# Optimization experiments

Hardware: AMD Instinct MI355X
Metric: run time of the kernel (lower is better)

The kernel has to match this reference:

```python
import jax, jax.numpy as jnp
import numpy as np

H = W = 64          # input_resolution
C = 256             # dim
HEADS = 8
WS = 8              # window_size
SHIFT = WS // 2
DEPTH = 2           # block 0: no shift, block 1: shifted + mask
HIDDEN = 4 * C      # mlp_ratio * dim
B = 8
N = WS * WS                 # tokens per window
NW = (H // WS) * (W // WS)  # windows per image
EPS = 1e-5


def _rel_pos_index():
    coords = np.stack(np.meshgrid(np.arange(WS), np.arange(WS), indexing='ij')).reshape(2, -1)
    rel = (coords[:, :, None] - coords[:, None, :]).transpose(1, 2, 0)
    rel[:, :, 0] += WS - 1
    rel[:, :, 1] += WS - 1
    rel[:, :, 0] *= 2 * WS - 1
    return rel.sum(-1)  # [N, N] indices into (2*ws-1)^2 table

REL_IDX = jnp.asarray(_rel_pos_index())


def _attn_mask():
    # Swin shift mask: label 3x3 regions, compare window-token labels
    img = np.zeros((H, W))
    slices = (slice(0, -WS), slice(-WS, -SHIFT), slice(-SHIFT, None))
    cnt = 0
    for hs in slices:
        for ws_ in slices:
            img[hs, ws_] = cnt
            cnt += 1
    mw = img.reshape(H // WS, WS, W // WS, WS).transpose(0, 2, 1, 3).reshape(-1, N)
    diff = mw[:, None, :] - mw[:, :, None]
    return jnp.asarray(np.where(diff != 0, -100.0, 0.0), dtype=np.float32)  # [nW, N, N]

ATTN_MASK = _attn_mask()


def layernorm(x, g, b):
    mu = jnp.mean(x, axis=-1, keepdims=True)
    var = jnp.mean((x - mu) ** 2, axis=-1, keepdims=True)
    return (x - mu) * jax.lax.rsqrt(var + EPS) * g + b


def setup_inputs() -> dict:
    key = jax.random.key(0)
    ks = jax.random.split(key, 6)
    s = 0.02
    return {
        'x': jax.random.normal(ks[0], (B, H * W, C), jnp.float32),
        'qkv_w': jax.random.normal(ks[1], (DEPTH, C, 3 * C), jnp.float32) * s,
        'qkv_b': jnp.zeros((DEPTH, 3 * C), jnp.float32),
        'proj_w': jax.random.normal(ks[2], (DEPTH, C, C), jnp.float32) * s,
        'proj_b': jnp.zeros((DEPTH, C), jnp.float32),
        'ln1_g': jnp.ones((DEPTH, C), jnp.float32),
        'ln1_b': jnp.zeros((DEPTH, C), jnp.float32),
        'ln2_g': jnp.ones((DEPTH, C), jnp.float32),
        'ln2_b': jnp.zeros((DEPTH, C), jnp.float32),
        'fc1_w': jax.random.normal(ks[3], (DEPTH, C, HIDDEN), jnp.float32) * s,
        'fc1_b': jnp.zeros((DEPTH, HIDDEN), jnp.float32),
        'fc2_w': jax.random.normal(ks[4], (DEPTH, HIDDEN, C), jnp.float32) * s,
        'fc2_b': jnp.zeros((DEPTH, C), jnp.float32),
        'rpb': jax.random.normal(ks[5], (DEPTH, (2 * WS - 1) ** 2, HEADS), jnp.float32) * s,
    }


def window_attention(xw, qw, qb, pw, pb, rpb_i, mask):
    # xw: [B*nW, N, C]
    B_ = xw.shape[0]
    d = C // HEADS
    qkv = (xw @ qw + qb).reshape(B_, N, 3, HEADS, d).transpose(2, 0, 3, 1, 4)
    q, k, v = qkv[0] * (d ** -0.5), qkv[1], qkv[2]   # [B_, h, N, d]
    attn = jnp.einsum('bhnd,bhmd->bhnm', q, k)
    bias = rpb_i[REL_IDX.reshape(-1)].reshape(N, N, HEADS).transpose(2, 0, 1)
    attn = attn + bias[None]
    if mask is not None:
        attn = attn.reshape(-1, NW, HEADS, N, N) + mask[None, :, None]
        attn = attn.reshape(-1, HEADS, N, N)
    attn = jax.nn.softmax(attn, axis=-1)
    out = jnp.einsum('bhnm,bhmd->bhnd', attn, v).transpose(0, 2, 1, 3).reshape(B_, N, C)
    return out @ pw + pb


def reference(x, qkv_w, qkv_b, proj_w, proj_b, ln1_g, ln1_b, ln2_g, ln2_b,
              fc1_w, fc1_b, fc2_w, fc2_b, rpb):
    for i in range(DEPTH):
        shift = 0 if i % 2 == 0 else SHIFT
        mask = None if shift == 0 else ATTN_MASK
        shortcut = x
        h = layernorm(x, ln1_g[i], ln1_b[i]).reshape(-1, H, W, C)
        if shift:
            h = jnp.roll(h, (-shift, -shift), axis=(1, 2))
        # window partition -> [B*nW, N, C]
        hw = h.reshape(-1, H // WS, WS, W // WS, WS, C).transpose(0, 1, 3, 2, 4, 5).reshape(-1, N, C)
        aw = window_attention(hw, qkv_w[i], qkv_b[i], proj_w[i], proj_b[i], rpb[i], mask)
        # window reverse
        h = aw.reshape(-1, H // WS, W // WS, WS, WS, C).transpose(0, 1, 3, 2, 4, 5).reshape(-1, H, W, C)
        if shift:
            h = jnp.roll(h, (shift, shift), axis=(1, 2))
        x = shortcut + h.reshape(-1, H * W, C)
        m = layernorm(x, ln2_g[i], ln2_b[i])
        m = jax.nn.gelu(m @ fc1_w[i] + fc1_b[i], approximate=False) @ fc2_w[i] + fc2_b[i]
        x = x + m
    return x
```

## Files before the change

### kernel.cpp

```cpp
#include <hip/hip_runtime.h>
#include <hip/hip_bf16.h>


typedef __hip_bfloat16 bf16;
typedef unsigned short u16;
typedef unsigned int u32;
typedef short short8 __attribute__((ext_vector_type(8)));
typedef float floatx4 __attribute__((ext_vector_type(4)));

#define DEVI static __device__ __forceinline__
#define WAITCNT_VM(n) asm volatile("s_waitcnt vmcnt(" #n ")" ::: "memory")

DEVI float lo16(u32 u) { union { u32 i; float f; } x; x.i = u << 16; return x.f; }
DEVI float hi16(u32 u) { union { u32 i; float f; } x; x.i = u & 0xffff0000u; return x.f; }
DEVI float b2f(u16 u) { union { u32 i; float f; } x; x.i = ((u32)u) << 16; return x.f; }
DEVI u16 f2b(float f) {
  union { float f; u32 i; } x; x.f = f;
  u32 r = x.i + 0x7fffu + ((x.i >> 16) & 1u);
  return (u16)(r >> 16);
}
DEVI float in_elem(const void* p, size_t i, int m) {
  return m ? b2f(((const u16*)p)[i]) : ((const float*)p)[i];
}
DEVI int swlab(int g) { return (g < 56) ? 0 : (g < 60 ? 1 : 2); }

DEVI float gelu_cheap(float v) {
  const float u = v * v;
  const float t = v * __builtin_fmaf(0.1029436f, u, 2.3022090f);
  const float e = __builtin_amdgcn_exp2f(t);
  const float r = __builtin_amdgcn_rcpf(e + 1.0f);
  return __builtin_fmaf(-v, r, v);
}

DEVI void async16(const bf16* g, bf16* l) {
  __builtin_amdgcn_global_load_lds((const __attribute__((address_space(1))) u32*)g,
                                   (__attribute__((address_space(3))) u32*)l, 16, 0, 0);
}

__global__ void k_detect(const u32* __restrict__ ln1g, int* __restrict__ mode) {
  if (threadIdx.x == 0 && blockIdx.x == 0)
    *mode = (ln1g[0] == 0x3F803F80u) ? 1 : 0;
}

__global__ __launch_bounds__(256) void k_ingest_ln(const void* __restrict__ xin,
    float* __restrict__ xf, const void* __restrict__ gamw, const void* __restrict__ betw,
    bf16* __restrict__ outp, const int* __restrict__ mode)
{
  const int m = *mode;
  const int l = threadIdx.x & 63, w = threadIdx.x >> 6;
  const int row = blockIdx.x * 4 + w;
  const int t = row & 63, win = row >> 6;
  const int bb = win >> 6, wi = win & 63;
  const int gh = ((wi >> 3) << 3) + (t >> 3);
  const int gw = ((wi & 7) << 3) + (t & 7);
  const int srow = (bb << 12) + (gh << 6) + gw;
  const int cb = l << 2;
  float4 v;
  if (m) {
    const uint2 u = *(const uint2*)((const u16*)xin + (size_t)srow * 256 + cb);
    v = make_float4(lo16(u.x), hi16(u.x), lo16(u.y), hi16(u.y));
  } else {
    v = ((const float4*)((const float*)xin + (size_t)srow * 256))[l];
  }
  ((float4*)(xf + (size_t)srow * 256))[l] = v;
  float s = v.x + v.y + v.z + v.w;
#pragma unroll
  for (int off = 32; off > 0; off >>= 1) s += __shfl_xor(s, off, 64);
  const float mu = s * 0.00390625f;
  const float a = v.x - mu, b = v.y - mu, c = v.z - mu, d = v.w - mu;
  float q = a * a + b * b + c * c + d * d;
#pragma unroll
  for (int off = 32; off > 0; off >>= 1) q += __shfl_xor(q, off, 64);
  const float rs = rsqrtf(q * 0.00390625f + 1e-5f);
  const float o0 = a * rs * in_elem(gamw, cb + 0, m) + in_elem(betw, cb + 0, m);
  const float o1 = b * rs * in_elem(gamw, cb + 1, m) + in_elem(betw, cb + 1, m);
  const float o2 = c * rs * in_elem(gamw, cb + 2, m) + in_elem(betw, cb + 2, m);
  const float o3 = d * rs * in_elem(gamw, cb + 3, m) + in_elem(betw, cb + 3, m);
  const u32 p0 = (u32)f2b(o0) | ((u32)f2b(o1) << 16);
  const u32 p1 = (u32)f2b(o2) | ((u32)f2b(o3) << 16);
  *(uint2*)((u16*)outp + (size_t)row * 256 + cb) = make_uint2(p0, p1);
}

__global__ __launch_bounds__(256) void k_transpose(
    const void* __restrict__ src, bf16* __restrict__ dst,
    const int* __restrict__ mode, int estride, int dstride, int R, int Cn) {
  __shared__ float T[32][33];
  const int m = *mode;
  const int tx = threadIdx.x & 31, ty = threadIdx.x >> 5;
  const int bc = blockIdx.x << 5, br = blockIdx.y << 5;
  for (int d = 0; d < 2; ++d) {
    __syncthreads();
#pragma unroll
    for (int dy = 0; dy < 4; ++dy) {
      const int r = br + ty + dy * 8;
      T[ty + dy * 8][tx] = in_elem(src, (size_t)d * estride + (size_t)r * Cn + bc + tx, m);
    }
    __syncthreads();
#pragma unroll
    for (int dy = 0; dy < 4; ++dy) {
      const int c = bc + ty + dy * 8;
      ((u16*)dst)[(size_t)d * dstride + (size_t)c * R + br + tx] = f2b(T[tx][ty + dy * 8]);
    }
  }
}

template <int EPI>
__global__ __launch_bounds__(256, 3) void k_gemm(
    const bf16* __restrict__ A, const bf16* __restrict__ Bt,
    const void* __restrict__ bias, bf16* __restrict__ outb,
    const int* __restrict__ mode, int boff, int K, int N)
{
  __shared__ __align__(16) bf16 As[3][128 * 32];
  __shared__ __align__(16) bf16 Bs[3][128 * 32];
  __shared__ __align__(16) float EPs[4][4][72];
  const int md = *mode;
  const int tid = threadIdx.x;
  const int l = tid & 63, wid = tid >> 6;
  const int wr = wid >> 1, wc = wid & 1;

  const int gx = gridDim.x;
  const int nwg = gx * gridDim.y;
  int fid = blockIdx.y * gx + blockIdx.x;
  if (!(nwg & 7)) fid = (fid & 7) * (nwg >> 3) + (fid >> 3);
  const int row0 = (fid / gx) * 128;
  const int col0 = (fid % gx) * 128;

  const int lrow = l >> 2;
  const int lkof = (((l & 3) ^ ((l >> 3) & 3)) * 8);
  const int qsw  = (((l >> 4) ^ ((l >> 1) & 3)) * 8);

  floatx4 acc[4][4];
#pragma unroll
  for (int mi = 0; mi < 4; ++mi)
#pragma unroll
    for (int ni = 0; ni < 4; ++ni)
      acc[mi][ni] = (floatx4){0.f, 0.f, 0.f, 0.f};

  auto stage = [&](int b, int kbase) {
    const int kk = kbase + lkof;
#pragma unroll
    for (int c = 0; c < 2; ++c) {
      const int seg = c * 4 + wid;
      async16(A + (size_t)(row0 + seg * 16 + lrow) * K + kk, &As[b][seg * 512]);
      async16(Bt + (size_t)(col0 + seg * 16 + lrow) * K + kk, &Bs[b][seg * 512]);
    }
  };

  const int nsl = K >> 5;
  stage(0, 0);
  stage(1, 32);

  for (int s = 0; s < nsl; ++s) {
    const int cur = s % 3;
    if (s < nsl - 1) { WAITCNT_VM(4); }
    else            { WAITCNT_VM(0); }
    __builtin_amdgcn_s_barrier();
    if (s + 2 < nsl) stage((s + 2) % 3, (s + 2) * 32);

    short8 af[4], bq[4];
#pragma unroll
    for (int mi = 0; mi < 4; ++mi)
      af[mi] = *(const short8*)&As[cur][(wr * 64 + mi * 16 + (l & 15)) * 32 + qsw];
#pragma unroll
    for (int ni = 0; ni < 4; ++ni)
      bq[ni] = *(const short8*)&Bs[cur][(wc * 64 + ni * 16 + (l & 15)) * 32 + qsw];
#pragma unroll
    for (int mi = 0; mi < 4; ++mi)
#pragma unroll
      for (int ni = 0; ni < 4; ++ni)
        acc[mi][ni] = __builtin_amdgcn_mfma_f32_16x16x32_bf16(af[mi], bq[ni], acc[mi][ni], 0, 0, 0);
  }

  float* EPw = &EPs[wid][0][0];
  const int cl = l & 15, rq = l >> 4;
  const int colb = wc * 64 + cl * 4;
  float bias4[4];
#pragma unroll
  for (int i = 0; i < 4; ++i) bias4[i] = in_elem(bias, (size_t)boff + col0 + colb + i, md);

#pragma unroll
  for (int mi = 0; mi < 4; ++mi) {
#pragma unroll
    for (int r = 0; r < 4; ++r) {
#pragma unroll
      for (int ni = 0; ni < 4; ++ni)
        EPw[rq * 72 + ni * 16 + cl] = acc[mi][ni][r];
      const float4 av = *(const float4*)&EPw[rq * 72 + cl * 4];
      float v0 = av.x + bias4[0], v1 = av.y + bias4[1];
      float v2 = av.z + bias4[2], v3 = av.w + bias4[3];
      if (EPI == 1) {
        v0 = gelu_cheap(v0); v1 = gelu_cheap(v1);
        v2 = gelu_cheap(v2); v3 = gelu_cheap(v3);
      }
      const int row = row0 + wr * 64 + mi * 16 + rq * 4 + r;
      const u32 p0 = (u32)f2b(v0) | ((u32)f2b(v1) << 16);
      const u32 p1 = (u32)f2b(v2) | ((u32)f2b(v3) << 16);
      *(uint2*)((u16*)outb + (size_t)row * N + col0 + colb) = make_uint2(p0, p1);
    }
  }
}

template <int MODE>
__global__ __launch_bounds__(256, 2) void k_fullN(
    const bf16* __restrict__ A, const bf16* __restrict__ Bt,
    const void* __restrict__ bias, const void* __restrict__ lng,
    const void* __restrict__ lnb, void* __restrict__ outp,
    float* __restrict__ xf, const int* __restrict__ mode,
    int boff, int lnoff, int K, int shift)
{
  __shared__ __align__(16) char smem[61440];
  bf16* As = (bf16*)smem;
  bf16* Bs = (bf16*)(smem + 12288);
  const int md = *mode;
  const int tid = threadIdx.x;
  const int l = tid & 63, w = tid >> 6;

  int fid = blockIdx.x;
  const int nwg = gridDim.x;
  if (!(nwg & 7)) fid = (fid & 7) * (nwg >> 3) + (fid >> 3);
  const int row0 = fid * 64;

  const int lrow = l >> 2;
  const int lkof = (((l & 3) ^ ((l >> 3) & 3)) * 8);
  const int qsw  = (((l >> 4) ^ ((l >> 1) & 3)) * 8);

  floatx4 acc[16];
#pragma unroll
  for (int ni = 0; ni < 16; ++ni) acc[ni] = (floatx4){0.f, 0.f, 0.f, 0.f};

  auto stage = [&](int b, int kbase) {
    const int kk = kbase + lkof;
    async16(A + (size_t)(row0 + w * 16 + lrow) * K + kk, As + b * 2048 + w * 512);
#pragma unroll
    for (int c = 0; c < 4; ++c) {
      const int seg = c * 4 + w;
      async16(Bt + (size_t)(seg * 16 + lrow) * K + kk, Bs + b * 8192 + seg * 512);
    }
  };

  const int nsl = K >> 5;
  stage(0, 0);
  stage(1, 32);

  for (int s = 0; s < nsl; ++s) {
    const int cur = s % 3;
    if (s < nsl - 1) { WAITCNT_VM(5); }
    else            { WAITCNT_VM(0); }
    __builtin_amdgcn_s_barrier();
    if (s + 2 < nsl) stage((s + 2) % 3, (s + 2) * 32);

    const short8 af = *(const short8*)&As[cur * 2048 + (w * 16 + (l & 15)) * 32 + qsw];
#pragma unroll
    for (int ni = 0; ni < 16; ++ni) {
      const short8 bq = *(const short8*)&Bs[cur * 8192 + (ni * 16 + (l & 15)) * 32 + qsw];
      acc[ni] = __builtin_amdgcn_mfma_f32_16x16x32_bf16(af, bq, acc[ni], 0, 0, 0);
    }
  }

  __syncthreads();

  float* EPw = (float*)smem + w * 1088;
  const int cl = l & 15, rq = l >> 4;
  const int c4 = l * 4;

  float bias4[4], g4[4], b4[4];
#pragma unroll
  for (int i = 0; i < 4; ++i) bias4[i] = in_elem(bias, (size_t)boff + c4 + i, md);
#pragma unroll
  for (int i = 0; i < 4; ++i) {
    g4[i] = in_elem(lng, (size_t)lnoff + c4 + i, md);
    b4[i] = in_elem(lnb, (size_t)lnoff + c4 + i, md);
  }

  for (int r = 0; r < 4; ++r) {
#pragma unroll
    for (int ni = 0; ni < 16; ++ni)
      EPw[rq * 272 + ni * 16 + cl] = acc[ni][r];

#pragma unroll
    for (int g = 0; g < 4; ++g) {
      const int lrow_g = row0 + w * 16 + g * 4 + r;
      const float4 av = *(const float4*)&EPw[g * 272 + c4];

      const int t_ = lrow_g & 63, win = lrow_g >> 6;
      const int bb = win >> 6, wi2 = win & 63;
      int gh = ((wi2 >> 3) << 3) + (t_ >> 3);
      int gw = ((wi2 & 7) << 3) + (t_ & 7);
      gh = (gh + shift) & 63; gw = (gw + shift) & 63;
      const int resrow = (bb << 12) + (gh << 6) + gw;
      const int dstrow = resrow;

      const float4 xv = *(const float4*)(xf + (size_t)resrow * 256 + c4);
      float t0 = av.x + bias4[0] + xv.x;
      float t1 = av.y + bias4[1] + xv.y;
      float t2 = av.z + bias4[2] + xv.z;
      float t3 = av.w + bias4[3] + xv.w;

      float s = t0 + t1 + t2 + t3;
#pragma unroll
      for (int off = 32; off > 0; off >>= 1) s += __shfl_xor(s, off, 64);
      const float mu = s * 0.00390625f;
      const float d0 = t0 - mu, d1 = t1 - mu, d2 = t2 - mu, d3 = t3 - mu;
      float q = d0 * d0 + d1 * d1 + d2 * d2 + d3 * d3;
#pragma unroll
      for (int off = 32; off > 0; off >>= 1) q += __shfl_xor(q, off, 64);
      const float rs = rsqrtf(q * 0.00390625f + 1e-5f);

      *(float4*)(xf + (size_t)resrow * 256 + c4) = make_float4(t0, t1, t2, t3);
      const u32 p0 = (u32)f2b(d0 * rs * g4[0] + b4[0]) | ((u32)f2b(d1 * rs * g4[1] + b4[1]) << 16);
      const u32 p1 = (u32)f2b(d2 * rs * g4[2] + b4[2]) | ((u32)f2b(d3 * rs * g4[3] + b4[3]) << 16);
      *(uint2*)((u16*)outp + (size_t)dstrow * 256 + c4) = make_uint2(p0, p1);
    }
  }
}

template <int MODE>
__global__ __launch_bounds__(256) void k_mlp(
    const bf16* __restrict__ A, const bf16* __restrict__ W1t, const bf16* __restrict__ W2t,
    const void* __restrict__ b1, const void* __restrict__ b2,
    const void* __restrict__ lng, const void* __restrict__ lnb,
    void* __restrict__ outp, float* __restrict__ xf, const int* __restrict__ mode,
    int b1off, int b2off, int lnoff)
{
  __shared__ __align__(16) char smem[81920];
  bf16* Al = (bf16*)smem;
  bf16* Wl = (bf16*)(smem + 32768);
  u16*  Hl = (u16*)(smem + 65536);
  const int md = *mode;
  const int tid = threadIdx.x;
  const int l = tid & 63, w = tid >> 6;
  int fid = blockIdx.x;
  const int nwg = gridDim.x;
  if (!(nwg & 7)) fid = (fid & 7) * (nwg >> 3) + (fid >> 3);
  const int row0 = fid * 64;

  const int lr4 = l >> 2;
  const int lkof = (((l & 3) ^ ((l >> 3) & 3)) * 8);
  const int qsw  = (((l >> 4) ^ ((l >> 1) & 3)) * 8);
  const int cl = l & 15, rq = l >> 4;

  floatx4 acc2[4][4];
#pragma unroll
  for (int mi = 0; mi < 4; ++mi)
#pragma unroll
    for (int ni = 0; ni < 4; ++ni)
      acc2[mi][ni] = (floatx4){0.f, 0.f, 0.f, 0.f};

  auto stageW1 = [&](int c, int s, int b) {
#pragma unroll
    for (int cc = 0; cc < 2; ++cc) {
      const int seg = w * 2 + cc;
      const size_t gr = (size_t)(c * 128 + seg * 16 + lr4) * 256;
      async16(W1t + gr + s * 32 + lkof,       Wl + b * 8192 + seg * 512);
      async16(W1t + gr + (s + 1) * 32 + lkof, Wl + b * 8192 + 4096 + seg * 512);
    }
  };
  auto stageW2 = [&](int c, int q, int b) {
#pragma unroll
    for (int cc = 0; cc < 4; ++cc) {
      const int seg = w * 4 + cc;
      async16(W2t + (size_t)(seg * 16 + lr4) * 1024 + c * 128 + q * 32 + lkof,
              Wl + b * 8192 + seg * 512);
    }
  };

#pragma unroll
  for (int s = 0; s < 8; ++s)
    async16(A + (size_t)(row0 + w * 16 + lr4) * 256 + s * 32 + lkof, Al + s * 2048 + w * 512);
  stageW1(0, 0, 0);

  int buf = 0;
  for (int c = 0; c < 8; ++c) {
    floatx4 acc1[4][2];
#pragma unroll
    for (int mi = 0; mi < 4; ++mi)
#pragma unroll
      for (int bni = 0; bni < 2; ++bni)
        acc1[mi][bni] = (floatx4){0.f, 0.f, 0.f, 0.f};

    for (int p = 0; p < 4; ++p) {
      __syncthreads();
      if (p < 3) stageW1(c, 2 * (p + 1), buf ^ 1);
      else       stageW2(c, 0, buf ^ 1);
#pragma unroll
      for (int h2 = 0; h2 < 2; ++h2) {
        const int ks = 2 * p + h2;
        short8 af[4];
#pragma unroll
        for (int mi = 0; mi < 4; ++mi)
          af[mi] = *(const short8*)&Al[ks * 2048 + (mi * 16 + cl) * 32 + qsw];
#pragma unroll
        for (int bni = 0; bni < 2; ++bni) {
          const short8 bq = *(const short8*)(Wl + buf * 8192 + h2 * 4096 +
                                             (w * 32 + bni * 16 + cl) * 32 + qsw);
#pragma unroll
          for (int mi = 0; mi < 4; ++mi)
            acc1[mi][bni] = __builtin_amdgcn_mfma_f32_16x16x32_bf16(af[mi], bq, acc1[mi][bni], 0, 0, 0);
        }
      }
      buf ^= 1;
    }

#pragma unroll
    for (int bni = 0; bni < 2; ++bni) {
      const int hcl = w * 32 + bni * 16 + cl;
      const float bv = in_elem(b1, (size_t)b1off + c * 128 + hcl, md);
      const int hq = (hcl >> 3) & 3, he = hcl & 7;
#pragma unroll
      for (int mi = 0; mi < 4; ++mi)
#pragma unroll
        for (int r = 0; r < 4; ++r) {
          const int hr = mi * 16 + rq * 4 + r;
          Hl[w * 2048 + hr * 32 + ((hq ^ ((hr >> 1) & 3)) * 8) + he] =
              f2b(gelu_cheap(acc1[mi][bni][r] + bv));
        }
    }

    for (int q = 0; q < 4; ++q) {
      __syncthreads();
      if (q < 3)      stageW2(c, q + 1, buf ^ 1);
      else if (c < 7) stageW1(c + 1, 0, buf ^ 1);
      short8 hf[4];
#pragma unroll
      for (int mi = 0; mi < 4; ++mi)
        hf[mi] = *(const short8*)((const bf16*)&Hl[q * 2048 + (mi * 16 + cl) * 32 + qsw]);
#pragma unroll
      for (int ni = 0; ni < 4; ++ni) {
        const short8 bq = *(const short8*)(Wl + buf * 8192 +
                                           (w * 64 + ni * 16 + cl) * 32 + qsw);
#pragma unroll
        for (int mi = 0; mi < 4; ++mi)
          acc2[mi][ni] = __builtin_amdgcn_mfma_f32_16x16x32_bf16(hf[mi], bq, acc2[mi][ni], 0, 0, 0);
      }
      buf ^= 1;
    }
  }

  __syncthreads();
  float* EPf = (float*)smem;
#pragma unroll
  for (int mi = 0; mi < 4; ++mi)
#pragma unroll
    for (int ni = 0; ni < 4; ++ni)
#pragma unroll
      for (int r = 0; r < 4; ++r)
        EPf[(mi * 16 + rq * 4 + r) * 272 + w * 64 + ni * 16 + cl] = acc2[mi][ni][r];
  __syncthreads();

  const int c4 = l * 4;
  float bias4[4], g4[4], b4[4];
#pragma unroll
  for (int i = 0; i < 4; ++i) bias4[i] = in_elem(b2, (size_t)b2off + c4 + i, md);
  if (MODE == 1) {
#pragma unroll
    for (int i = 0; i < 4; ++i) {
      g4[i] = in_elem(lng, (size_t)lnoff + c4 + i, md);
      b4[i] = in_elem(lnb, (size_t)lnoff + c4 + i, md);
    }
  }

  for (int rr = 0; rr < 16; ++rr) {
    const int lrow_g = row0 + w * 16 + rr;
    const float4 av = *(const float4*)&EPf[(w * 16 + rr) * 272 + c4];
    const float4 xv = *(const float4*)(xf + (size_t)lrow_g * 256 + c4);
    float t0 = av.x + bias4[0] + xv.x;
    float t1 = av.y + bias4[1] + xv.y;
    float t2 = av.z + bias4[2] + xv.z;
    float t3 = av.w + bias4[3] + xv.w;

    if (MODE == 2) {
      *(float4*)((float*)outp + (size_t)lrow_g * 256 + c4) = make_float4(t0, t1, t2, t3);
      continue;
    }

    const int bb = lrow_g >> 12, th = (lrow_g >> 6) & 63, tw = lrow_g & 63;
    const int gh = (th + 60) & 63, gw = (tw + 60) & 63;
    const int wi2 = ((gh >> 3) << 3) + (gw >> 3);
    const int tt = ((gh & 7) << 3) + (gw & 7);
    const int dstrow = (bb << 12) + (wi2 << 6) + tt;

    float s = t0 + t1 + t2 + t3;
#pragma unroll
    for (int off = 32; off > 0; off >>= 1) s += __shfl_xor(s, off, 64);
    const float mu = s * 0.00390625f;
    const float d0 = t0 - mu, d1 = t1 - mu, d2 = t2 - mu, d3 = t3 - mu;
    float q = d0 * d0 + d1 * d1 + d2 * d2 + d3 * d3;
#pragma unroll
    for (int off = 32; off > 0; off >>= 1) q += __shfl_xor(q, off, 64);
    const float rs = rsqrtf(q * 0.00390625f + 1e-5f);

    *(float4*)(xf + (size_t)lrow_g * 256 + c4) = make_float4(t0, t1, t2, t3);
    const u32 p0 = (u32)f2b(d0 * rs * g4[0] + b4[0]) | ((u32)f2b(d1 * rs * g4[1] + b4[1]) << 16);
    const u32 p1 = (u32)f2b(d2 * rs * g4[2] + b4[2]) | ((u32)f2b(d3 * rs * g4[3] + b4[3]) << 16);
    *(uint2*)((u16*)outp + (size_t)dstrow * 256 + c4) = make_uint2(p0, p1);
  }
}

__global__ __launch_bounds__(256, 2) void k_attn(
    const bf16* __restrict__ qkv, const void* __restrict__ rpb,
    bf16* __restrict__ outp, const int* __restrict__ mode, int eoff, int shifted)
{
  __shared__ __align__(16) u16 Pl[4][64][72];
  __shared__ __align__(16) u16 Vt[4][32][72];
  __shared__ float rpbs[4][228];
  const int md = *mode;
  const int l = threadIdx.x & 63, w = threadIdx.x >> 6;
  const int cl = l & 15, qd = l >> 4;
  const int ko = qd * 8;
  const int win = blockIdx.x;
  const int wi = win & 63;
  const int whb = (wi >> 3) << 3, wwb = (wi & 7) << 3;
  const size_t rowbase = (size_t)win * 64 * 768;

  for (int hh = 0; hh < 2; ++hh) {
    const int h = w + hh * 4;
    for (int i = l; i < 225; i += 64)
      rpbs[w][i] = in_elem(rpb, (size_t)eoff + (size_t)i * 8 + h, md);
    {
      const u16* vrow = (const u16*)(qkv + rowbase + (size_t)l * 768 + 512 + h * 32);
#pragma unroll
      for (int n = 0; n < 32; ++n) Vt[w][n][l] = vrow[n];
    }
    short8 qf[4], kf[4];
#pragma unroll
    for (int t = 0; t < 4; ++t) {
      qf[t] = *(const short8*)(qkv + rowbase + (size_t)(t * 16 + cl) * 768 + h * 32 + ko);
      kf[t] = *(const short8*)(qkv + rowbase + (size_t)(t * 16 + cl) * 768 + 256 + h * 32 + ko);
    }
    __syncthreads();

    floatx4 S[4][4];
#pragma unroll
    for (int mi = 0; mi < 4; ++mi)
#pragma unroll
      for (int ni = 0; ni < 4; ++ni)
        S[mi][ni] = __builtin_amdgcn_mfma_f32_16x16x32_bf16(qf[mi], kf[ni], (floatx4){0.f, 0.f, 0.f, 0.f}, 0, 0, 0);

    int cty[4], ctx[4], clab[4];
#pragma unroll
    for (int ni = 0; ni < 4; ++ni) {
      const int ct = ni * 16 + cl;
      cty[ni] = ct >> 3; ctx[ni] = ct & 7;
      clab[ni] = shifted ? (swlab(whb + cty[ni]) * 3 + swlab(wwb + ctx[ni])) : 0;
    }

    float invs[4][4];
#pragma unroll
    for (int mi = 0; mi < 4; ++mi) {
#pragma unroll
      for (int r = 0; r < 4; ++r) {
        const int rt = mi * 16 + qd * 4 + r;
        const int rty = rt >> 3, rtx = rt & 7;
        const int rlab = shifted ? (swlab(whb + rty) * 3 + swlab(wwb + rtx)) : 0;
        float sv[4];
#pragma unroll
        for (int ni = 0; ni < 4; ++ni) {
          float x = S[mi][ni][r] * 0.17677669529663687f;
          x += rpbs[w][(rty - cty[ni] + 7) * 15 + (rtx - ctx[ni] + 7)];
          if (shifted && (rlab != clab[ni])) x -= 100.f;
          sv[ni] = x;
        }
        float mx = fmaxf(fmaxf(sv[0], sv[1]), fmaxf(sv[2], sv[3]));
        mx = fmaxf(mx, __shfl_xor(mx, 1, 64));
        mx = fmaxf(mx, __shfl_xor(mx, 2, 64));
        mx = fmaxf(mx, __shfl_xor(mx, 4, 64));
        mx = fmaxf(mx, __shfl_xor(mx, 8, 64));
        float sum = 0.f;
#pragma unroll
        for (int ni = 0; ni < 4; ++ni) { sv[ni] = __expf(sv[ni] - mx); sum += sv[ni]; }
        sum += __shfl_xor(sum, 1, 64);
        sum += __shfl_xor(sum, 2, 64);
        sum += __shfl_xor(sum, 4, 64);
        sum += __shfl_xor(sum, 8, 64);
        invs[mi][r] = __builtin_amdgcn_rcpf(sum);
#pragma unroll
        for (int ni = 0; ni < 4; ++ni) Pl[w][rt][ni * 16 + cl] = f2b(sv[ni]);
      }
    }
    __syncthreads();

    floatx4 O[4][2];
#pragma unroll
    for (int mi = 0; mi < 4; ++mi)
#pragma unroll
      for (int nv = 0; nv < 2; ++nv)
        O[mi][nv] = (floatx4){0.f, 0.f, 0.f, 0.f};
    short8 vf[2][2];
#pragma unroll
    for (int nv = 0; nv < 2; ++nv)
#pragma unroll
      for (int kk = 0; kk < 2; ++kk)
        vf[nv][kk] = *(const short8*)&Vt[w][nv * 16 + cl][kk * 32 + ko];
#pragma unroll
    for (int mi = 0; mi < 4; ++mi) {
      const short8 pf0 = *(const short8*)&Pl[w][mi * 16 + cl][ko];
      const short8 pf1 = *(const short8*)&Pl[w][mi * 16 + cl][32 + ko];
#pragma unroll
      for (int nv = 0; nv < 2; ++nv) {
        O[mi][nv] = __builtin_amdgcn_mfma_f32_16x16x32_bf16(pf0, vf[nv][0], O[mi][nv], 0, 0, 0);
        O[mi][nv] = __builtin_amdgcn_mfma_f32_16x16x32_bf16(pf1, vf[nv][1], O[mi][nv], 0, 0, 0);
      }
    }

#pragma unroll
    for (int mi = 0; mi < 4; ++mi)
#pragma unroll
      for (int nv = 0; nv < 2; ++nv)
#pragma unroll
        for (int r = 0; r < 4; ++r) {
          const int row = mi * 16 + qd * 4 + r;
          ((u16*)outp)[((size_t)win * 64 + row) * 256 + h * 32 + nv * 16 + cl] =
              f2b(O[mi][nv][r] * invs[mi][r]);
        }
    __syncthreads();
  }
}

extern "C" void kernel_launch(void* const* d_in, const int* in_sizes, int n_in,
                              void* d_out, int out_size, void* d_ws, size_t ws_size,
                              hipStream_t stream) {
  (void)in_sizes; (void)n_in; (void)out_size; (void)ws_size;
  const void* x_in   = d_in[0];
  const void* qkv_w  = d_in[1];
  const void* qkv_b  = d_in[2];
  const void* proj_w = d_in[3];
  const void* proj_b = d_in[4];
  const void* ln1_g  = d_in[5];
  const void* ln1_b  = d_in[6];
  const void* ln2_g  = d_in[7];
  const void* ln2_b  = d_in[8];
  const void* fc1_w  = d_in[9];
  const void* fc1_b  = d_in[10];
  const void* fc2_w  = d_in[11];
  const void* fc2_b  = d_in[12];
  const void* rpb    = d_in[13];

  char* ws = (char*)d_ws;
  float* xf  = (float*)ws;
  bf16* bufQ = (bf16*)(ws + 100663296);
  bf16* bufB = (bf16*)(ws + 150994944);
  bf16* wT   = (bf16*)(ws + 167772160);
  int* mode  = (int*)(ws + 170917888);

  k_detect<<<1, 1, 0, stream>>>((const u32*)ln1_g, mode);
  k_ingest_ln<<<8192, 256, 0, stream>>>(x_in, xf, ln1_g, ln1_b, bufB, mode);

  k_transpose<<<dim3(24, 8), 256, 0, stream>>>(qkv_w,  wT,          mode, 196608, 786432, 256, 768);
  k_transpose<<<dim3(8, 8), 256, 0, stream>>>(proj_w, wT + 196608, mode, 65536, 786432, 256, 256);
  k_transpose<<<dim3(32, 8), 256, 0, stream>>>(fc1_w, wT + 262144, mode, 262144, 786432, 256, 1024);
  k_transpose<<<dim3(8, 32), 256, 0, stream>>>(fc2_w, wT + 524288, mode, 262144, 786432, 1024, 256);

  for (int i = 0; i < 2; ++i) {
    const int shift = i ? 4 : 0;
    bf16* base  = wT + (size_t)i * 786432;
    bf16* qkvT  = base;
    bf16* projT = base + 196608;
    bf16* fc1T  = base + 262144;
    bf16* fc2T  = base + 524288;

    k_gemm<0><<<dim3(6, 256), 256, 0, stream>>>(bufB, qkvT, qkv_b, bufQ, mode, i * 768, 256, 768);
    k_attn<<<512, 256, 0, stream>>>(bufQ, rpb, bufB, mode, i * 1800, i);
    k_fullN<0><<<512, 256, 0, stream>>>(bufB, projT, proj_b, ln2_g, ln2_b, bufQ, xf, mode,
                                        i * 256, i * 256, 256, shift);
    if (i == 0)
      k_mlp<1><<<512, 256, 0, stream>>>(bufQ, fc1T, fc2T, fc1_b, fc2_b, ln1_g, ln1_b,
                                        bufB, xf, mode, 0, 0, 256);
    else
      k_mlp<2><<<512, 256, 0, stream>>>(bufQ, fc1T, fc2T, fc1_b, fc2_b, nullptr, nullptr,
                                        d_out, xf, mode, 1024, 256, 0);
  }
}
```

Before: 399.0 us.

## Enlarge MLP tile to 128 rows with 8 waves and triple-buffered weight staging

The fused MLP kernel now processes 128 rows per workgroup with 512 threads, split as two row halves by four column quarters. Each staged fc1/fc2 weight tile is therefore reused across twice as many rows. Weight staging moves from double buffering with __syncthreads to a three-slot ring that prefetches two steps ahead, using explicit vmcnt waits and raw s_barrier. The cost is 144KB of LDS per block, which allows one block per CU, and a grid of only 256 blocks.

```diff
diff --git a/kernel.cpp b/kernel.cpp
--- a/kernel.cpp
+++ b/kernel.cpp
@@ -315,24 +315,25 @@
 }
 
 template <int MODE>
-__global__ __launch_bounds__(256) void k_mlp(
+__global__ __launch_bounds__(512, 2) void k_mlp(
     const bf16* __restrict__ A, const bf16* __restrict__ W1t, const bf16* __restrict__ W2t,
     const void* __restrict__ b1, const void* __restrict__ b2,
     const void* __restrict__ lng, const void* __restrict__ lnb,
     void* __restrict__ outp, float* __restrict__ xf, const int* __restrict__ mode,
     int b1off, int b2off, int lnoff)
 {
-  __shared__ __align__(16) char smem[81920];
+  __shared__ __align__(16) char smem[147456];
   bf16* Al = (bf16*)smem;
-  bf16* Wl = (bf16*)(smem + 32768);
-  u16*  Hl = (u16*)(smem + 65536);
+  bf16* Wl = (bf16*)(smem + 65536);
+  u16*  Hl = (u16*)(smem + 114688);
   const int md = *mode;
   const int tid = threadIdx.x;
   const int l = tid & 63, w = tid >> 6;
+  const int rh = w >> 2, wq = w & 3;
   int fid = blockIdx.x;
   const int nwg = gridDim.x;
   if (!(nwg & 7)) fid = (fid & 7) * (nwg >> 3) + (fid >> 3);
-  const int row0 = fid * 64;
+  const int row0 = fid * 128;
 
   const int lr4 = l >> 2;
   const int lkof = (((l & 3) ^ ((l >> 3) & 3)) * 8);
@@ -347,29 +348,31 @@
       acc2[mi][ni] = (floatx4){0.f, 0.f, 0.f, 0.f};
 
   auto stageW1 = [&](int c, int s, int b) {
+    const size_t gr = (size_t)(c * 128 + w * 16 + lr4) * 256;
+    async16(W1t + gr + s * 32 + lkof,       Wl + b * 8192 + w * 512);
+    async16(W1t + gr + (s + 1) * 32 + lkof, Wl + b * 8192 + 4096 + w * 512);
+  };
+  auto stageW2 = [&](int c, int q, int b) {
 #pragma unroll
     for (int cc = 0; cc < 2; ++cc) {
       const int seg = w * 2 + cc;
-      const size_t gr = (size_t)(c * 128 + seg * 16 + lr4) * 256;
-      async16(W1t + gr + s * 32 + lkof,       Wl + b * 8192 + seg * 512);
-      async16(W1t + gr + (s + 1) * 32 + lkof, Wl + b * 8192 + 4096 + seg * 512);
-    }
-  };
-  auto stageW2 = [&](int c, int q, int b) {
-#pragma unroll
-    for (int cc = 0; cc < 4; ++cc) {
-      const int seg = w * 4 + cc;
       async16(W2t + (size_t)(seg * 16 + lr4) * 1024 + c * 128 + q * 32 + lkof,
               Wl + b * 8192 + seg * 512);
     }
   };
+  auto stage_g = [&](int g) {
+    const int c = g >> 3, sub = g & 7, b = g % 3;
+    if (sub < 4) stageW1(c, 2 * sub, b);
+    else         stageW2(c, sub - 4, b);
+  };
 
 #pragma unroll
   for (int s = 0; s < 8; ++s)
-    async16(A + (size_t)(row0 + w * 16 + lr4) * 256 + s * 32 + lkof, Al + s * 2048 + w * 512);
-  stageW1(0, 0, 0);
-
-  int buf = 0;
+    async16(A + (size_t)(row0 + w * 16 + lr4) * 256 + s * 32 + lkof, Al + s * 4096 + w * 512);
+  stage_g(0);
+  stage_g(1);
+
+  int ph = 0;
   for (int c = 0; c < 8; ++c) {
     floatx4 acc1[4][2];
 #pragma unroll
@@ -378,61 +381,64 @@
       for (int bni = 0; bni < 2; ++bni)
         acc1[mi][bni] = (floatx4){0.f, 0.f, 0.f, 0.f};
 
-    for (int p = 0; p < 4; ++p) {
-      __syncthreads();
-      if (p < 3) stageW1(c, 2 * (p + 1), buf ^ 1);
-      else       stageW2(c, 0, buf ^ 1);
+    for (int p = 0; p < 4; ++p, ++ph) {
+      if (ph < 63) { WAITCNT_VM(2); }
+      else         { WAITCNT_VM(0); }
+      __builtin_amdgcn_s_barrier();
+      if (ph + 2 < 64) stage_g(ph + 2);
+      const int buf = ph % 3;
 #pragma unroll
       for (int h2 = 0; h2 < 2; ++h2) {
         const int ks = 2 * p + h2;
         short8 af[4];
 #pragma unroll
         for (int mi = 0; mi < 4; ++mi)
-          af[mi] = *(const short8*)&Al[ks * 2048 + (mi * 16 + cl) * 32 + qsw];
+          af[mi] = *(const short8*)&Al[ks * 4096 + (rh * 64 + mi * 16 + cl) * 32 + qsw];
 #pragma unroll
         for (int bni = 0; bni < 2; ++bni) {
           const short8 bq = *(const short8*)(Wl + buf * 8192 + h2 * 4096 +
-                                             (w * 32 + bni * 16 + cl) * 32 + qsw);
+                                             (wq * 32 + bni * 16 + cl) * 32 + qsw);
 #pragma unroll
           for (int mi = 0; mi < 4; ++mi)
             acc1[mi][bni] = __builtin_amdgcn_mfma_f32_16x16x32_bf16(af[mi], bq, acc1[mi][bni], 0, 0, 0);
         }
       }
-      buf ^= 1;
     }
 
 #pragma unroll
     for (int bni = 0; bni < 2; ++bni) {
-      const int hcl = w * 32 + bni * 16 + cl;
-      const float bv = in_elem(b1, (size_t)b1off + c * 128 + hcl, md);
-      const int hq = (hcl >> 3) & 3, he = hcl & 7;
+      const int h32 = bni * 16 + cl;
+      const float bv = in_elem(b1, (size_t)b1off + c * 128 + wq * 32 + h32, md);
+      const int hq = h32 >> 3, he = h32 & 7;
 #pragma unroll
       for (int mi = 0; mi < 4; ++mi)
 #pragma unroll
         for (int r = 0; r < 4; ++r) {
-          const int hr = mi * 16 + rq * 4 + r;
-          Hl[w * 2048 + hr * 32 + ((hq ^ ((hr >> 1) & 3)) * 8) + he] =
+          const int hr = rh * 64 + mi * 16 + rq * 4 + r;
+          Hl[wq * 4096 + hr * 32 + ((hq ^ ((hr >> 1) & 3)) * 8) + he] =
               f2b(gelu_cheap(acc1[mi][bni][r] + bv));
         }
     }
-
-    for (int q = 0; q < 4; ++q) {
-      __syncthreads();
-      if (q < 3)      stageW2(c, q + 1, buf ^ 1);
-      else if (c < 7) stageW1(c + 1, 0, buf ^ 1);
+    asm volatile("s_waitcnt lgkmcnt(0)" ::: "memory");
+
+    for (int q = 0; q < 4; ++q, ++ph) {
+      if (ph < 63) { WAITCNT_VM(2); }
+      else         { WAITCNT_VM(0); }
+      __builtin_amdgcn_s_barrier();
+      if (ph + 2 < 64) stage_g(ph + 2);
+      const int buf = ph % 3;
       short8 hf[4];
 #pragma unroll
       for (int mi = 0; mi < 4; ++mi)
-        hf[mi] = *(const short8*)((const bf16*)&Hl[q * 2048 + (mi * 16 + cl) * 32 + qsw]);
+        hf[mi] = *(const short8*)((const bf16*)&Hl[q * 4096 + (rh * 64 + mi * 16 + cl) * 32 + qsw]);
 #pragma unroll
       for (int ni = 0; ni < 4; ++ni) {
         const short8 bq = *(const short8*)(Wl + buf * 8192 +
-                                           (w * 64 + ni * 16 + cl) * 32 + qsw);
+                                           (wq * 64 + ni * 16 + cl) * 32 + qsw);
 #pragma unroll
         for (int mi = 0; mi < 4; ++mi)
           acc2[mi][ni] = __builtin_amdgcn_mfma_f32_16x16x32_bf16(hf[mi], bq, acc2[mi][ni], 0, 0, 0);
       }
-      buf ^= 1;
     }
   }
 
@@ -444,7 +450,7 @@
     for (int ni = 0; ni < 4; ++ni)
 #pragma unroll
       for (int r = 0; r < 4; ++r)
-        EPf[(mi * 16 + rq * 4 + r) * 272 + w * 64 + ni * 16 + cl] = acc2[mi][ni][r];
+        EPf[(rh * 64 + mi * 16 + rq * 4 + r) * 272 + wq * 64 + ni * 16 + cl] = acc2[mi][ni][r];
   __syncthreads();
 
   const int c4 = l * 4;
@@ -663,10 +669,10 @@
     k_fullN<0><<<512, 256, 0, stream>>>(bufB, projT, proj_b, ln2_g, ln2_b, bufQ, xf, mode,
                                         i * 256, i * 256, 256, shift);
     if (i == 0)
-      k_mlp<1><<<512, 256, 0, stream>>>(bufQ, fc1T, fc2T, fc1_b, fc2_b, ln1_g, ln1_b,
+      k_mlp<1><<<256, 512, 0, stream>>>(bufQ, fc1T, fc2T, fc1_b, fc2_b, ln1_g, ln1_b,
                                         bufB, xf, mode, 0, 0, 256);
     else
-      k_mlp<2><<<512, 256, 0, stream>>>(bufQ, fc1T, fc2T, fc1_b, fc2_b, nullptr, nullptr,
+      k_mlp<2><<<256, 512, 0, stream>>>(bufQ, fc1T, fc2T, fc1_b, fc2_b, nullptr, nullptr,
                                         d_out, xf, mode, 1024, 256, 0);
   }
 }
```

After: 391.4 us. Within noise of the previous version (-1.9%).
